# Kernel optimization log

Hardware: AMD Instinct MI355X
Metric: run time of the kernel (lower is better)

The kernel has to match this reference:

```python
import jax, jax.numpy as jnp
import numpy as np

ALPHA = 0.5
NUM_CLASSES = 86
FEAT = 256
N = 131072


def setup_inputs() -> dict:
    key = jax.random.key(0)
    k1, k2, k3 = jax.random.split(key, 3)
    features = jax.random.normal(k1, (N, FEAT), dtype=jnp.float32)
    labels = jax.random.randint(k2, (N,), 0, NUM_CLASSES)
    # non-trainable centers buffer, RandomNormal init (stddev 0.05 like keras default)
    centers = 0.05 * jax.random.normal(k3, (NUM_CLASSES, FEAT), dtype=jnp.float32)
    return {"features": features, "labels": labels, "centers": centers}


def reference(features, labels, centers):
    labels = labels.reshape(-1)
    # gather per-sample centers: [N, F]
    centers_batch = centers[labels]
    d = features - centers_batch
    # tf.nn.l2_loss = 0.5 * sum(x^2)
    loss = 0.5 * jnp.sum(d * d)
    # appear_times via unique_with_counts == per-class occurrence count gathered back
    counts = jax.ops.segment_sum(
        jnp.ones((labels.shape[0],), dtype=jnp.float32), labels,
        num_segments=NUM_CLASSES)  # [C]
    appear_times = counts[labels][:, None]  # [N, 1]
    diff = ALPHA * (-d) / (1.0 + appear_times)  # (centers_batch - features) scaled
    # tf.scatter_sub accumulates duplicate indices
    new_centers = centers.at[labels].add(-diff)
    return loss, new_centers
```

## Files before the change

### kernel.cpp

```cpp
#include <hip/hip_runtime.h>

#define ALPHA 0.5f
#define NCLS 86
#define FEAT 256
#define NTOT 131072

constexpr int K   = 64;
constexpr int CH  = NTOT / K;
constexpr int L4  = CH / 4;

constexpr size_t WS_S   = 0;
constexpr size_t WS_CNT = (size_t)NCLS * K * FEAT;
constexpr size_t WS_L2  = WS_CNT + (size_t)NCLS * K;
constexpr size_t WS_CLS = WS_L2 + (size_t)NCLS * K;

__global__ __launch_bounds__(128) void ctc_main(
    const float4* __restrict__ feat4, const int4* __restrict__ lab4,
    float4* __restrict__ S_part4, float* __restrict__ cnt_part,
    float* __restrict__ l2_part)
{
    const int wave = threadIdx.x >> 6;
    const int lane = threadIdx.x & 63;
    const int pair = blockIdx.x * 2 + wave;
    const int k = pair % K;
    const int c = pair / K;
    const int base = k * CH;

    const int4* lp = lab4 + base / 4 + lane;

    float4 acc = {0.f, 0.f, 0.f, 0.f};
    float  acc2 = 0.f;
    int    cnt  = 0;

    int4 L = lp[0];
    for (int it = 0; it < L4; it += 64) {
        const int4 Lc = L;
        if (it + 64 < L4) L = lp[it + 64];
        unsigned long long m0 = __ballot(Lc.x == c);
        unsigned long long m1 = __ballot(Lc.y == c);
        unsigned long long m2 = __ballot(Lc.z == c);
        unsigned long long m3 = __ballot(Lc.w == c);
        cnt += __popcll(m0) + __popcll(m1) + __popcll(m2) + __popcll(m3);
#define ACCUM(v)                                                           \
        { acc.x += v.x; acc.y += v.y; acc.z += v.z; acc.w += v.w;          \
          acc2  += v.x * v.x + v.y * v.y + v.z * v.z + v.w * v.w; }
#define DRAIN(mm, j)                                                       \
        while (mm) {                                                       \
            const int b0 = (int)__ffsll((long long)mm) - 1; mm &= mm - 1;  \
            if (mm) {                                                      \
                const int b1 = (int)__ffsll((long long)mm) - 1;            \
                mm &= mm - 1;                                              \
                const float4 v0 =                                          \
                    feat4[(size_t)(base + (it + b0) * 4 + j) * 64 + lane]; \
                const float4 v1 =                                          \
                    feat4[(size_t)(base + (it + b1) * 4 + j) * 64 + lane]; \
                ACCUM(v0) ACCUM(v1)                                        \
            } else {                                                       \
                const float4 v0 =                                          \
                    feat4[(size_t)(base + (it + b0) * 4 + j) * 64 + lane]; \
                ACCUM(v0)                                                  \
            }                                                              \
        }
        DRAIN(m0, 0) DRAIN(m1, 1) DRAIN(m2, 2) DRAIN(m3, 3)
#undef DRAIN
#undef ACCUM
    }

    S_part4[(size_t)pair * 64 + lane] = acc;

    for (int off = 32; off; off >>= 1)
        acc2 += __shfl_down(acc2, off, 64);
    if (lane == 0) {
        cnt_part[pair] = (float)cnt;
        l2_part[pair]  = acc2;
    }
}

__global__ __launch_bounds__(256) void ctc_finalize(
    const float* __restrict__ centers, const float* __restrict__ S_part,
    const float* __restrict__ cnt_part, const float* __restrict__ l2_part,
    float* __restrict__ class_loss, float* __restrict__ out_centers)
{
    const int c = blockIdx.x;
    const int t = threadIdx.x;

    float S = 0.f;
    for (int k = 0; k < K; ++k)
        S += S_part[((size_t)c * K + k) * FEAT + t];

    __shared__ float sn, sl2;
    if (t == 0) {
        float a = 0.f, b = 0.f;
        for (int k = 0; k < K; ++k) {
            a += cnt_part[c * K + k];
            b += l2_part[c * K + k];
        }
        sn = a; sl2 = b;
    }
    __syncthreads();

    const float n  = sn;
    const float cc = centers[c * FEAT + t];
    out_centers[c * FEAT + t] = cc + ALPHA * (S - n * cc) / (1.f + n);

    float part = 0.5f * n * cc * cc - S * cc;
    for (int off = 32; off; off >>= 1) part += __shfl_down(part, off, 64);

    __shared__ float red[4];
    const int wv = t >> 6, ln = t & 63;
    if (ln == 0) red[wv] = part;
    __syncthreads();
    if (t == 0)
        class_loss[c] = red[0] + red[1] + red[2] + red[3] + 0.5f * sl2;
}

__global__ void ctc_loss_write(const float* __restrict__ class_loss,
                               float* __restrict__ out)
{
    const int l = threadIdx.x;
    float v = (l < NCLS) ? class_loss[l] : 0.f;
    if (l + 64 < NCLS) v += class_loss[l + 64];
    for (int off = 32; off; off >>= 1) v += __shfl_down(v, off, 64);
    if (l == 0) out[0] = v;
}

extern "C" void kernel_launch(void* const* d_in, const int* in_sizes, int n_in,
                              void* d_out, int out_size, void* d_ws, size_t ws_size,
                              hipStream_t stream)
{
    const float* feat    = (const float*)d_in[0];
    const int*   labels  = (const int*)d_in[1];
    const float* centers = (const float*)d_in[2];
    float* out = (float*)d_out;
    float* ws  = (float*)d_ws;

    float* S_part     = ws + WS_S;
    float* cnt_part   = ws + WS_CNT;
    float* l2_part    = ws + WS_L2;
    float* class_loss = ws + WS_CLS;

    ctc_main<<<NCLS * K / 2, 128, 0, stream>>>(
        (const float4*)feat, (const int4*)labels,
        (float4*)S_part, cnt_part, l2_part);

    ctc_finalize<<<NCLS, 256, 0, stream>>>(
        centers, S_part, cnt_part, l2_part, class_loss, out + 1);

    ctc_loss_write<<<1, 64, 0, stream>>>(class_loss, out);
}
```

Before: 34.02 us.

## Compact matching sample indices into LDS lists and batch feature gathers

The main kernel now scans all labels for its chunk up front, loading 8 label vectors at once, and uses ballot prefix counts to write matching sample indices into a per-wave shared-memory list. It then drains the list with batched nontemporal loads of 4, 2 and 1 rows, instead of walking ballot masks serially while loading labels. This is meant to raise memory-level parallelism on the feature gather. The finalize kernel now splits the 64-way partial reduction across 1024 threads and uses a wave shuffle for the counts. In exchange it adds LDS use and scatter writes, and it sets an occupancy hint on the main kernel.

```diff
diff --git a/kernel.cpp b/kernel.cpp
--- a/kernel.cpp
+++ b/kernel.cpp
@@ -5,113 +5,140 @@
 #define FEAT 256
 #define NTOT 131072
 
-constexpr int K   = 64;
-constexpr int CH  = NTOT / K;
-constexpr int L4  = CH / 4;
+constexpr int K    = 64;
+constexpr int CH   = NTOT / K;
+constexpr int LCAP = 512;
+
+typedef float vf4 __attribute__((ext_vector_type(4)));
 
 constexpr size_t WS_S   = 0;
 constexpr size_t WS_CNT = (size_t)NCLS * K * FEAT;
 constexpr size_t WS_L2  = WS_CNT + (size_t)NCLS * K;
 constexpr size_t WS_CLS = WS_L2 + (size_t)NCLS * K;
 
-__global__ __launch_bounds__(128) void ctc_main(
-    const float4* __restrict__ feat4, const int4* __restrict__ lab4,
-    float4* __restrict__ S_part4, float* __restrict__ cnt_part,
+template<int W>
+__device__ __forceinline__ void gatherW(const vf4* __restrict__ feat4,
+                                        const int* wl, int i, int lane,
+                                        vf4& acc, float& acc2)
+{
+    vf4 v[W];
+#pragma unroll
+    for (int j = 0; j < W; ++j)
+        v[j] = __builtin_nontemporal_load(&feat4[(size_t)wl[i + j] * 64 + lane]);
+#pragma unroll
+    for (int j = 0; j < W; ++j) {
+        acc += v[j];
+        acc2 += v[j].x * v[j].x + v[j].y * v[j].y
+              + v[j].z * v[j].z + v[j].w * v[j].w;
+    }
+}
+
+__global__ __launch_bounds__(128, 6) void ctc_main(
+    const vf4* __restrict__ feat4, const int4* __restrict__ lab4,
+    vf4* __restrict__ S_part4, float* __restrict__ cnt_part,
     float* __restrict__ l2_part)
 {
+    __shared__ int list[2][LCAP];
     const int wave = threadIdx.x >> 6;
     const int lane = threadIdx.x & 63;
     const int pair = blockIdx.x * 2 + wave;
     const int k = pair % K;
     const int c = pair / K;
     const int base = k * CH;
+    int* wl = list[wave];
 
-    const int4* lp = lab4 + base / 4 + lane;
+    const int4* lp = lab4 + (base >> 2) + lane;
+    const unsigned long long ltm = ((unsigned long long)1 << lane) - 1;
 
-    float4 acc = {0.f, 0.f, 0.f, 0.f};
-    float  acc2 = 0.f;
-    int    cnt  = 0;
+    vf4 acc = {0.f, 0.f, 0.f, 0.f};
+    float acc2 = 0.f;
+    int total = 0, nl = 0;
 
-    int4 L = lp[0];
-    for (int it = 0; it < L4; it += 64) {
-        const int4 Lc = L;
-        if (it + 64 < L4) L = lp[it + 64];
-        unsigned long long m0 = __ballot(Lc.x == c);
-        unsigned long long m1 = __ballot(Lc.y == c);
-        unsigned long long m2 = __ballot(Lc.z == c);
-        unsigned long long m3 = __ballot(Lc.w == c);
-        cnt += __popcll(m0) + __popcll(m1) + __popcll(m2) + __popcll(m3);
-#define ACCUM(v)                                                           \
-        { acc.x += v.x; acc.y += v.y; acc.z += v.z; acc.w += v.w;          \
-          acc2  += v.x * v.x + v.y * v.y + v.z * v.z + v.w * v.w; }
-#define DRAIN(mm, j)                                                       \
-        while (mm) {                                                       \
-            const int b0 = (int)__ffsll((long long)mm) - 1; mm &= mm - 1;  \
-            if (mm) {                                                      \
-                const int b1 = (int)__ffsll((long long)mm) - 1;            \
-                mm &= mm - 1;                                              \
-                const float4 v0 =                                          \
-                    feat4[(size_t)(base + (it + b0) * 4 + j) * 64 + lane]; \
-                const float4 v1 =                                          \
-                    feat4[(size_t)(base + (it + b1) * 4 + j) * 64 + lane]; \
-                ACCUM(v0) ACCUM(v1)                                        \
-            } else {                                                       \
-                const float4 v0 =                                          \
-                    feat4[(size_t)(base + (it + b0) * 4 + j) * 64 + lane]; \
-                ACCUM(v0)                                                  \
-            }                                                              \
+    auto drain = [&]() {
+        int i = 0;
+        for (; i + 4 <= nl; i += 4) gatherW<4>(feat4, wl, i, lane, acc, acc2);
+        if (i + 2 <= nl) { gatherW<2>(feat4, wl, i, lane, acc, acc2); i += 2; }
+        if (i < nl)        gatherW<1>(feat4, wl, i, lane, acc, acc2);
+        nl = 0;
+    };
+
+    for (int h = 0; h < 2; ++h) {
+        int4 Lr[4];
+#pragma unroll
+        for (int q = 0; q < 4; ++q) Lr[q] = lp[(h * 4 + q) * 64];
+#pragma unroll
+        for (int q = 0; q < 4; ++q) {
+            const int4 Lc = Lr[q];
+            const int sbase = base + ((h * 4 + q) * 64 + lane) * 4;
+            unsigned long long m0 = __ballot(Lc.x == c);
+            unsigned long long m1 = __ballot(Lc.y == c);
+            unsigned long long m2 = __ballot(Lc.z == c);
+            unsigned long long m3 = __ballot(Lc.w == c);
+            const int c0 = __popcll(m0), c1 = __popcll(m1);
+            const int c2 = __popcll(m2), c3 = __popcll(m3);
+            if (Lc.x == c) wl[nl + __popcll(m0 & ltm)]           = sbase;
+            if (Lc.y == c) wl[nl + c0 + __popcll(m1 & ltm)]      = sbase + 1;
+            if (Lc.z == c) wl[nl + c0 + c1 + __popcll(m2 & ltm)] = sbase + 2;
+            if (Lc.w == c) wl[nl + c0 + c1 + c2 + __popcll(m3 & ltm)] = sbase + 3;
+            const int add = c0 + c1 + c2 + c3;
+            nl += add; total += add;
+            if (nl > LCAP - 256) drain();
         }
-        DRAIN(m0, 0) DRAIN(m1, 1) DRAIN(m2, 2) DRAIN(m3, 3)
-#undef DRAIN
-#undef ACCUM
     }
+    drain();
 
     S_part4[(size_t)pair * 64 + lane] = acc;
 
     for (int off = 32; off; off >>= 1)
         acc2 += __shfl_down(acc2, off, 64);
     if (lane == 0) {
-        cnt_part[pair] = (float)cnt;
+        cnt_part[pair] = (float)total;
         l2_part[pair]  = acc2;
     }
 }
 
-__global__ __launch_bounds__(256) void ctc_finalize(
+__global__ __launch_bounds__(1024) void ctc_finalize(
     const float* __restrict__ centers, const float* __restrict__ S_part,
     const float* __restrict__ cnt_part, const float* __restrict__ l2_part,
     float* __restrict__ class_loss, float* __restrict__ out_centers)
 {
-    const int c = blockIdx.x;
-    const int t = threadIdx.x;
+    const int c  = blockIdx.x;
+    const int t  = threadIdx.x & 255;
+    const int kq = threadIdx.x >> 8;
 
     float S = 0.f;
-    for (int k = 0; k < K; ++k)
-        S += S_part[((size_t)c * K + k) * FEAT + t];
+#pragma unroll
+    for (int j = 0; j < 16; ++j)
+        S += S_part[((size_t)c * K + kq * 16 + j) * FEAT + t];
 
-    __shared__ float sn, sl2;
-    if (t == 0) {
-        float a = 0.f, b = 0.f;
-        for (int k = 0; k < K; ++k) {
-            a += cnt_part[c * K + k];
-            b += l2_part[c * K + k];
+    __shared__ float red[4][FEAT];
+    __shared__ float r2[4];
+    __shared__ float sn_s, sl2_s;
+    red[kq][t] = S;
+
+    if (threadIdx.x < 64) {
+        float a = cnt_part[c * K + threadIdx.x];
+        float b = l2_part[c * K + threadIdx.x];
+        for (int off = 32; off; off >>= 1) {
+            a += __shfl_down(a, off, 64);
+            b += __shfl_down(b, off, 64);
         }
-        sn = a; sl2 = b;
+        if (threadIdx.x == 0) { sn_s = a; sl2_s = b; }
     }
     __syncthreads();
 
-    const float n  = sn;
-    const float cc = centers[c * FEAT + t];
-    out_centers[c * FEAT + t] = cc + ALPHA * (S - n * cc) / (1.f + n);
-
-    float part = 0.5f * n * cc * cc - S * cc;
-    for (int off = 32; off; off >>= 1) part += __shfl_down(part, off, 64);
-
-    __shared__ float red[4];
-    const int wv = t >> 6, ln = t & 63;
-    if (ln == 0) red[wv] = part;
+    if (threadIdx.x < 256) {
+        const float Sf = red[0][t] + red[1][t] + red[2][t] + red[3][t];
+        const float n  = sn_s;
+        const float cc = centers[c * FEAT + t];
+        out_centers[c * FEAT + t] = cc + ALPHA * (Sf - n * cc) / (1.f + n);
+        float part = 0.5f * n * cc * cc - Sf * cc;
+        for (int off = 32; off; off >>= 1) part += __shfl_down(part, off, 64);
+        if ((t & 63) == 0) r2[t >> 6] = part;
+    }
     __syncthreads();
-    if (t == 0)
-        class_loss[c] = red[0] + red[1] + red[2] + red[3] + 0.5f * sl2;
+    if (threadIdx.x == 0)
+        class_loss[c] = r2[0] + r2[1] + r2[2] + r2[3] + 0.5f * sl2_s;
 }
 
 __global__ void ctc_loss_write(const float* __restrict__ class_loss,
@@ -140,10 +167,10 @@
     float* class_loss = ws + WS_CLS;
 
     ctc_main<<<NCLS * K / 2, 128, 0, stream>>>(
-        (const float4*)feat, (const int4*)labels,
-        (float4*)S_part, cnt_part, l2_part);
+        (const vf4*)feat, (const int4*)labels,
+        (vf4*)S_part, cnt_part, l2_part);
 
-    ctc_finalize<<<NCLS, 256, 0, stream>>>(
+    ctc_finalize<<<NCLS, 1024, 0, stream>>>(
         centers, S_part, cnt_part, l2_part, class_loss, out + 1);
 
     ctc_loss_write<<<1, 64, 0, stream>>>(class_loss, out);
```

Result: slower. 42.15 us (+23.9%).

## Interleave per-lane-slot feature loads and split finalize reduction across four k-groups

Applied to the files above, without the earlier changes.

The main kernel's drain loop now walks all four ballot masks together, issuing up to four feature row loads per iteration. Slots with no remaining bits load from a valid dummy address and discard the value, which exposes more memory-level parallelism than draining each mask on its own. The finalize kernel grows to 1024 threads: four groups each sum 16 of the 64 partials, the results are combined through shared memory, and the count and l2 partials are reduced with wave shuffles instead of a serial loop on one thread. The costs are redundant dummy loads and extra shared-memory traffic and synchronisation.

```diff
diff --git a/kernel.cpp b/kernel.cpp
--- a/kernel.cpp
+++ b/kernel.cpp
@@ -5,9 +5,9 @@
 #define FEAT 256
 #define NTOT 131072
 
-constexpr int K   = 64;
-constexpr int CH  = NTOT / K;
-constexpr int L4  = CH / 4;
+constexpr int K  = 64;
+constexpr int CH = NTOT / K;
+constexpr int L4 = CH / 4;
 
 constexpr size_t WS_S   = 0;
 constexpr size_t WS_CNT = (size_t)NCLS * K * FEAT;
@@ -26,7 +26,8 @@
     const int c = pair / K;
     const int base = k * CH;
 
-    const int4* lp = lab4 + base / 4 + lane;
+    const int4* lp = lab4 + (base >> 2) + lane;
+    const size_t dummy = (size_t)base * 64 + lane;
 
     float4 acc = {0.f, 0.f, 0.f, 0.f};
     float  acc2 = 0.f;
@@ -41,28 +42,26 @@
         unsigned long long m2 = __ballot(Lc.z == c);
         unsigned long long m3 = __ballot(Lc.w == c);
         cnt += __popcll(m0) + __popcll(m1) + __popcll(m2) + __popcll(m3);
+
 #define ACCUM(v)                                                           \
         { acc.x += v.x; acc.y += v.y; acc.z += v.z; acc.w += v.w;          \
           acc2  += v.x * v.x + v.y * v.y + v.z * v.z + v.w * v.w; }
-#define DRAIN(mm, j)                                                       \
-        while (mm) {                                                       \
-            const int b0 = (int)__ffsll((long long)mm) - 1; mm &= mm - 1;  \
-            if (mm) {                                                      \
-                const int b1 = (int)__ffsll((long long)mm) - 1;            \
-                mm &= mm - 1;                                              \
-                const float4 v0 =                                          \
-                    feat4[(size_t)(base + (it + b0) * 4 + j) * 64 + lane]; \
-                const float4 v1 =                                          \
-                    feat4[(size_t)(base + (it + b1) * 4 + j) * 64 + lane]; \
-                ACCUM(v0) ACCUM(v1)                                        \
-            } else {                                                       \
-                const float4 v0 =                                          \
-                    feat4[(size_t)(base + (it + b0) * 4 + j) * 64 + lane]; \
-                ACCUM(v0)                                                  \
-            }                                                              \
+        while (m0 | m1 | m2 | m3) {
+            const bool h0 = m0 != 0, h1 = m1 != 0, h2 = m2 != 0, h3 = m3 != 0;
+            const int b0 = (int)__ffsll((long long)m0) - 1;
+            const int b1 = (int)__ffsll((long long)m1) - 1;
+            const int b2 = (int)__ffsll((long long)m2) - 1;
+            const int b3 = (int)__ffsll((long long)m3) - 1;
+            m0 &= m0 - 1; m1 &= m1 - 1; m2 &= m2 - 1; m3 &= m3 - 1;
+            const float4 v0 = feat4[h0 ? (size_t)(base + (it + b0) * 4 + 0) * 64 + lane : dummy];
+            const float4 v1 = feat4[h1 ? (size_t)(base + (it + b1) * 4 + 1) * 64 + lane : dummy];
+            const float4 v2 = feat4[h2 ? (size_t)(base + (it + b2) * 4 + 2) * 64 + lane : dummy];
+            const float4 v3 = feat4[h3 ? (size_t)(base + (it + b3) * 4 + 3) * 64 + lane : dummy];
+            if (h0) ACCUM(v0)
+            if (h1) ACCUM(v1)
+            if (h2) ACCUM(v2)
+            if (h3) ACCUM(v3)
         }
-        DRAIN(m0, 0) DRAIN(m1, 1) DRAIN(m2, 2) DRAIN(m3, 3)
-#undef DRAIN
 #undef ACCUM
     }
 
@@ -76,42 +75,48 @@
     }
 }
 
-__global__ __launch_bounds__(256) void ctc_finalize(
+__global__ __launch_bounds__(1024) void ctc_finalize(
     const float* __restrict__ centers, const float* __restrict__ S_part,
     const float* __restrict__ cnt_part, const float* __restrict__ l2_part,
     float* __restrict__ class_loss, float* __restrict__ out_centers)
 {
-    const int c = blockIdx.x;
-    const int t = threadIdx.x;
+    const int c  = blockIdx.x;
+    const int t  = threadIdx.x & 255;
+    const int kq = threadIdx.x >> 8;
 
     float S = 0.f;
-    for (int k = 0; k < K; ++k)
-        S += S_part[((size_t)c * K + k) * FEAT + t];
+#pragma unroll
+    for (int j = 0; j < 16; ++j)
+        S += S_part[((size_t)c * K + kq * 16 + j) * FEAT + t];
 
-    __shared__ float sn, sl2;
-    if (t == 0) {
-        float a = 0.f, b = 0.f;
-        for (int k = 0; k < K; ++k) {
-            a += cnt_part[c * K + k];
-            b += l2_part[c * K + k];
+    __shared__ float red[4][FEAT];
+    __shared__ float r2[4];
+    __shared__ float sn_s, sl2_s;
+    red[kq][t] = S;
+
+    if (threadIdx.x < 64) {
+        float a = cnt_part[c * K + threadIdx.x];
+        float b = l2_part[c * K + threadIdx.x];
+        for (int off = 32; off; off >>= 1) {
+            a += __shfl_down(a, off, 64);
+            b += __shfl_down(b, off, 64);
         }
-        sn = a; sl2 = b;
+        if (threadIdx.x == 0) { sn_s = a; sl2_s = b; }
     }
     __syncthreads();
 
-    const float n  = sn;
-    const float cc = centers[c * FEAT + t];
-    out_centers[c * FEAT + t] = cc + ALPHA * (S - n * cc) / (1.f + n);
-
-    float part = 0.5f * n * cc * cc - S * cc;
-    for (int off = 32; off; off >>= 1) part += __shfl_down(part, off, 64);
-
-    __shared__ float red[4];
-    const int wv = t >> 6, ln = t & 63;
-    if (ln == 0) red[wv] = part;
+    if (threadIdx.x < 256) {
+        const float Sf = red[0][t] + red[1][t] + red[2][t] + red[3][t];
+        const float n  = sn_s;
+        const float cc = centers[c * FEAT + t];
+        out_centers[c * FEAT + t] = cc + ALPHA * (Sf - n * cc) / (1.f + n);
+        float part = 0.5f * n * cc * cc - Sf * cc;
+        for (int off = 32; off; off >>= 1) part += __shfl_down(part, off, 64);
+        if ((t & 63) == 0) r2[t >> 6] = part;
+    }
     __syncthreads();
-    if (t == 0)
-        class_loss[c] = red[0] + red[1] + red[2] + red[3] + 0.5f * sl2;
+    if (threadIdx.x == 0)
+        class_loss[c] = r2[0] + r2[1] + r2[2] + r2[3] + 0.5f * sl2_s;
 }
 
 __global__ void ctc_loss_write(const float* __restrict__ class_loss,
@@ -143,7 +148,7 @@
         (const float4*)feat, (const int4*)labels,
         (float4*)S_part, cnt_part, l2_part);
 
-    ctc_finalize<<<NCLS, 256, 0, stream>>>(
+    ctc_finalize<<<NCLS, 1024, 0, stream>>>(
         centers, S_part, cnt_part, l2_part, class_loss, out + 1);
 
     ctc_loss_write<<<1, 64, 0, stream>>>(class_loss, out);
```

New measurement: 32.68 us, median of 2. -3.9%, faster.
